# Optimization experiments

Hardware: AMD Instinct MI355X
Metric: run time of the kernel (lower is better)

Reference implementation:

```python
import jax, jax.numpy as jnp
import numpy as np

NUM_HEADS = 8


def setup_inputs() -> dict:
    key = jax.random.key(0)
    ks = jax.random.split(key, 16)
    B, Ct, Co, H, W = 1, 256, 128, 64, 64
    s = lambda k, *shape: jax.random.normal(k, shape, dtype=jnp.float32) * 0.02
    return {
        "thermal_features": jax.random.normal(ks[0], (B, Ct, H, W), dtype=jnp.float32),
        "optical_features": jax.random.normal(ks[1], (B, Co, H, W), dtype=jnp.float32),
        "emissivity_map": jax.random.uniform(ks[2], (B, 1, H, W), dtype=jnp.float32),
        "Wq": s(ks[3], Ct, Ct), "bq": jnp.zeros((Ct,), jnp.float32),
        "Wk": s(ks[4], Ct, Co), "bk": jnp.zeros((Ct,), jnp.float32),
        "Wv": s(ks[5], Ct, Co), "bv": jnp.zeros((Ct,), jnp.float32),
        "conv1_w": s(ks[6], 32, 1, 3, 3), "conv1_b": jnp.zeros((32,), jnp.float32),
        "conv2_w": s(ks[7], NUM_HEADS, 32, 1, 1), "conv2_b": jnp.zeros((NUM_HEADS,), jnp.float32),
        "Wp": s(ks[8], Ct, Ct), "bp": jnp.zeros((Ct,), jnp.float32),
    }


def reference(thermal_features, optical_features, emissivity_map,
              Wq, bq, Wk, bk, Wv, bv, conv1_w, conv1_b, conv2_w, conv2_b, Wp, bp):
    B, Ct, H, W = thermal_features.shape
    Co = optical_features.shape[1]
    N = H * W
    h = NUM_HEADS
    d = Ct // h
    scale = d ** (-0.5)

    # flatten spatial -> tokens: [B, N, C]
    t_flat = thermal_features.reshape(B, Ct, N).transpose(0, 2, 1)
    o_flat = optical_features.reshape(B, Co, N).transpose(0, 2, 1)

    # projections, split heads: [B, h, N, d]
    q = (t_flat @ Wq.T + bq).reshape(B, N, h, d).transpose(0, 2, 1, 3)
    k = (o_flat @ Wk.T + bk).reshape(B, N, h, d).transpose(0, 2, 1, 3)
    v = (o_flat @ Wv.T + bv).reshape(B, N, h, d).transpose(0, 2, 1, 3)

    # full attention scores: [B, h, N, N]
    attn = jnp.einsum('bhqd,bhkd->bhqk', q, k) * scale

    # emissivity gate: Conv(1->32, 3x3, pad 1) -> ReLU -> Conv(32->h, 1x1) -> Sigmoid
    g = jax.lax.conv_general_dilated(emissivity_map, conv1_w, (1, 1), 'SAME',
                                     dimension_numbers=('NCHW', 'OIHW', 'NCHW'))
    g = jax.nn.relu(g + conv1_b[None, :, None, None])
    g = jax.lax.conv_general_dilated(g, conv2_w, (1, 1), 'SAME',
                                     dimension_numbers=('NCHW', 'OIHW', 'NCHW'))
    g = jax.nn.sigmoid(g + conv2_b[None, :, None, None])  # [B, h, H, W]
    g = g.reshape(B, h, N)[..., None]  # [B, h, N, 1] gates query rows

    attn = jax.nn.softmax(attn * g, axis=-1)  # dropout is identity in eval

    out = jnp.einsum('bhqk,bhkd->bhqd', attn, v)  # [B, h, N, d]
    out = out.transpose(0, 2, 1, 3).reshape(B, N, Ct)
    out = out @ Wp.T + bp
    return out.transpose(0, 2, 1).reshape(B, Ct, H, W)
```

## Files before the change

### kernel.cpp

```cpp
#include <hip/hip_runtime.h>
#include <hip/hip_bf16.h>

#define N_TOK 4096
#define CT 256

typedef __attribute__((ext_vector_type(8))) short bf16x8;
typedef __attribute__((ext_vector_type(16))) float f32x16;

__device__ __forceinline__ unsigned pkbf(float a, float b) {
  float2 t; t.x = a; t.y = b;
  __hip_bfloat162 h = __float22bfloat162_rn(t);
  return *reinterpret_cast<unsigned*>(&h);
}

#if __has_builtin(__builtin_amdgcn_exp2f)
__device__ __forceinline__ float fexp2(float x) { return __builtin_amdgcn_exp2f(x); }
#else
__device__ __forceinline__ float fexp2(float x) { return exp2f(x); }
#endif

__global__ __launch_bounds__(256) void prep_kernel(
    const float* __restrict__ thermal, const float* __restrict__ optical,
    const float* __restrict__ Wq, const float* __restrict__ Wk,
    const float* __restrict__ Wv, const float* __restrict__ Wp,
    const float* __restrict__ em, const float* __restrict__ w1,
    const float* __restrict__ b1, const float* __restrict__ w2,
    const float* __restrict__ b2,
    unsigned short* __restrict__ Xbt, unsigned short* __restrict__ Xbo,
    unsigned short* __restrict__ Wall, float* __restrict__ g)
{
  __shared__ unsigned short tile[64][264];
  const int bx = blockIdx.x, tid = threadIdx.x;
  if (bx < 128) {
    const bool th = (bx < 64);
    const float* X = th ? thermal : optical;
    unsigned short* Xb = th ? Xbt : Xbo;
    const int CIN = th ? 256 : 128;
    const int n0 = (th ? bx : bx - 64) * 64;
    const int nl = tid & 63;
    const int cw = (tid >> 6) * 4;
    for (int c0 = 0; c0 < CIN; c0 += 16) {
      int c = c0 + cw;
      float x0 = X[(size_t)(c + 0) * N_TOK + n0 + nl];
      float x1 = X[(size_t)(c + 1) * N_TOK + n0 + nl];
      float x2 = X[(size_t)(c + 2) * N_TOK + n0 + nl];
      float x3 = X[(size_t)(c + 3) * N_TOK + n0 + nl];
      uint2 w; w.x = pkbf(x0, x1); w.y = pkbf(x2, x3);
      *(uint2*)&tile[nl][c] = w;
    }
    __syncthreads();
    const int n = tid >> 2, q = tid & 3;
    const int cb = q * (CIN / 4);
    for (int j = 0; j < CIN / 4; j += 4)
      *(uint2*)(Xb + (size_t)(n0 + n) * CIN + cb + j) = *(const uint2*)&tile[n][cb + j];
  } else if (bx < 224) {
    int i = (bx - 128) * 2048 + tid * 8;
    const float* src; int off;
    if (i < 65536)       { src = Wq; off = 0; }
    else if (i < 98304)  { src = Wk; off = 65536; }
    else if (i < 131072) { src = Wv; off = 98304; }
    else                 { src = Wp; off = 131072; }
    float4 f0 = *(const float4*)(src + (i - off));
    float4 f1 = *(const float4*)(src + (i - off) + 4);
    uint4 o;
    o.x = pkbf(f0.x, f0.y); o.y = pkbf(f0.z, f0.w);
    o.z = pkbf(f1.x, f1.y); o.w = pkbf(f1.z, f1.w);
    *(uint4*)(Wall + i) = o;
  } else {
    int n = (bx - 224) * 256 + tid;
    int y = n >> 6, x = n & 63;
    float e[9];
#pragma unroll
    for (int dy = 0; dy < 3; dy++)
#pragma unroll
      for (int dx = 0; dx < 3; dx++) {
        int yy = y + dy - 1, xx = x + dx - 1;
        e[dy * 3 + dx] = (yy >= 0 && yy < 64 && xx >= 0 && xx < 64)
                             ? em[yy * 64 + xx] : 0.f;
      }
    float c1[32];
#pragma unroll
    for (int oc = 0; oc < 32; oc++) {
      float a = b1[oc];
#pragma unroll
      for (int t = 0; t < 9; t++) a = fmaf(e[t], w1[oc * 9 + t], a);
      c1[oc] = fmaxf(a, 0.f);
    }
#pragma unroll
    for (int hh = 0; hh < 8; hh++) {
      float a = b2[hh];
#pragma unroll
      for (int oc = 0; oc < 32; oc++) a = fmaf(c1[oc], w2[hh * 32 + oc], a);
      g[hh * N_TOK + n] = 1.f / (1.f + __expf(-a));
    }
  }
}

template <int CIN>
__device__ __forceinline__ void gemm_tile(
    const unsigned short* __restrict__ xp, const unsigned short* __restrict__ wp,
    f32x16& accE, f32x16& accO)
{
#pragma unroll
  for (int c = 0; c < CIN; c += 32) {
    bf16x8 a0 = *(const bf16x8*)(xp + c);
    bf16x8 b0 = *(const bf16x8*)(wp + c);
    bf16x8 a1 = *(const bf16x8*)(xp + c + 16);
    bf16x8 b1 = *(const bf16x8*)(wp + c + 16);
    accE = __builtin_amdgcn_mfma_f32_32x32x16_bf16(a0, b0, accE, 0, 0, 0);
    accO = __builtin_amdgcn_mfma_f32_32x32x16_bf16(a1, b1, accO, 0, 0, 0);
  }
}

__global__ __launch_bounds__(256) void qkv_kernel(
    const unsigned short* __restrict__ Xbt, const unsigned short* __restrict__ Xbo,
    const unsigned short* __restrict__ Wall,
    const float* __restrict__ bq, const float* __restrict__ bk,
    const float* __restrict__ bv, const float* __restrict__ g,
    unsigned short* __restrict__ Qh, unsigned short* __restrict__ Kh,
    unsigned short* __restrict__ Vf)
{
  __shared__ float ldsT[4][32][33];
  const int tid = threadIdx.x;
  const int wave = tid >> 6, lane = tid & 63;
  const int l31 = lane & 31, hi = lane >> 5;
  const int y = blockIdx.y;
  const int head = y & 7;
  const int n0 = blockIdx.x * 128 + wave * 32;

  f32x16 accE, accO;
#pragma unroll
  for (int i = 0; i < 16; i++) { accE[i] = 0.f; accO[i] = 0.f; }
  float bo;
  if (y < 8) {
    gemm_tile<256>(Xbt + (size_t)(n0 + l31) * 256 + hi * 8,
                   Wall + (size_t)(head * 32 + l31) * 256 + hi * 8, accE, accO);
    bo = bq[head * 32 + l31];
  } else if (y < 16) {
    gemm_tile<128>(Xbo + (size_t)(n0 + l31) * 128 + hi * 8,
                   Wall + 65536 + (size_t)(head * 32 + l31) * 128 + hi * 8, accE, accO);
    bo = bk[head * 32 + l31];
  } else {
    gemm_tile<128>(Xbo + (size_t)(n0 + l31) * 128 + hi * 8,
                   Wall + 98304 + (size_t)(head * 32 + l31) * 128 + hi * 8, accE, accO);
    bo = bv[head * 32 + l31];
  }
  float val[16];
#pragma unroll
  for (int r = 0; r < 16; r++) val[r] = accE[r] + accO[r] + bo;

  if (y < 8) {
    const float QSC = 0.17677669529663689f * 1.4426950408889634f;
#pragma unroll
    for (int r = 0; r < 16; r++) {
      int t = n0 + (r & 3) + 8 * (r >> 2) + 4 * hi;
      val[r] *= QSC * g[head * N_TOK + t];
    }
  }
#pragma unroll
  for (int r = 0; r < 16; r++)
    ldsT[wave][(r & 3) + 8 * (r >> 2) + 4 * hi][l31] = val[r];

  if (y < 16) {
    unsigned pk[8];
#pragma unroll
    for (int i = 0; i < 8; i++)
      pk[i] = pkbf(ldsT[wave][l31][16 * hi + 2 * i],
                   ldsT[wave][l31][16 * hi + 2 * i + 1]);
    unsigned short* dst = (y < 8 ? Qh : Kh) +
        ((size_t)head * N_TOK + n0 + l31) * 32 + 16 * hi;
    *(uint4*)dst = make_uint4(pk[0], pk[1], pk[2], pk[3]);
    *(uint4*)(dst + 8) = make_uint4(pk[4], pk[5], pk[6], pk[7]);
  } else {
    unsigned pk[8];
#pragma unroll
    for (int i = 0; i < 8; i++)
      pk[i] = pkbf(ldsT[wave][16 * hi + 2 * i][l31],
                   ldsT[wave][16 * hi + 2 * i + 1][l31]);
    unsigned short* dst = Vf +
        (((size_t)head * 256 + (n0 >> 4) + hi) * 32 + l31) * 16;
    *(uint4*)dst = make_uint4(pk[0], pk[1], pk[2], pk[3]);
    *(uint4*)(dst + 8) = make_uint4(pk[4], pk[5], pk[6], pk[7]);
  }
}

__global__ __launch_bounds__(256, 4) void attn_kernel(
    const unsigned short* __restrict__ Qh, const unsigned short* __restrict__ Kh,
    const unsigned short* __restrict__ Vf, unsigned short* __restrict__ Ab)
{
  __shared__ float combA[4][32][33];
  __shared__ float combL[4][32];
  const int tid = threadIdx.x;
  const int wave = tid >> 6, lane = tid & 63;
  const int l31 = lane & 31, hi = lane >> 5;
  const int hh = blockIdx.x >> 7;
  const int qb = blockIdx.x & 127;
  const int qrow0 = qb * 32;
  const int kbase0 = wave * 1024;

  const unsigned short* qrow = Qh + ((size_t)hh * N_TOK + qrow0 + l31) * 32;
  const bf16x8 qf0 = *(const bf16x8*)(qrow + hi * 8);
  const bf16x8 qf1 = *(const bf16x8*)(qrow + 16 + hi * 8);

  const unsigned short* kb_base = Kh + (size_t)hh * (N_TOK * 32);
  const unsigned short* vf_base = Vf + (size_t)hh * (256 * 32 * 16);

  f32x16 acc, zero16;
#pragma unroll
  for (int i = 0; i < 16; i++) { acc[i] = 0.f; zero16[i] = 0.f; }
  float lsum = 0.f;

#define LK(kb, s) (*(const bf16x8*)(kb_base + (size_t)((kb) + l31) * 32 + (s) * 16 + hi * 8))
#define LV(kt2)   (*(const bf16x8*)(vf_base + (size_t)((kt2) * 32 + l31) * 16 + hi * 8))

  bf16x8 kf0 = LK(kbase0, 0), kf1 = LK(kbase0, 1);
  bf16x8 vb0 = LV(kbase0 >> 4), vb1 = LV((kbase0 >> 4) + 1);

#pragma unroll 2
  for (int kt = 0; kt < 1024; kt += 32) {
    const int nxt = (kt + 32 < 1024) ? (kbase0 + kt + 32) : kbase0;
    bf16x8 nk0 = LK(nxt, 0), nk1 = LK(nxt, 1);
    bf16x8 nv0 = LV(nxt >> 4), nv1 = LV((nxt >> 4) + 1);

    f32x16 s = __builtin_amdgcn_mfma_f32_32x32x16_bf16(kf0, qf0, zero16, 0, 0, 0);
    s = __builtin_amdgcn_mfma_f32_32x32x16_bf16(kf1, qf1, s, 0, 0, 0);

    float p[16];
#pragma unroll
    for (int r = 0; r < 16; r++) p[r] = fexp2(s[r]);

    lsum += (((p[0] + p[1]) + (p[2] + p[3])) + ((p[4] + p[5]) + (p[6] + p[7]))) +
            (((p[8] + p[9]) + (p[10] + p[11])) + ((p[12] + p[13]) + (p[14] + p[15])));

    unsigned a0 = pkbf(p[0], p[1]),   a1 = pkbf(p[2], p[3]);
    unsigned b0 = pkbf(p[4], p[5]),   b1 = pkbf(p[6], p[7]);
    unsigned c0 = pkbf(p[8], p[9]),   c1 = pkbf(p[10], p[11]);
    unsigned d0 = pkbf(p[12], p[13]), d1 = pkbf(p[14], p[15]);
    asm("v_permlane32_swap_b32 %0, %1" : "+v"(a0), "+v"(b0));
    asm("v_permlane32_swap_b32 %0, %1" : "+v"(a1), "+v"(b1));
    asm("v_permlane32_swap_b32 %0, %1" : "+v"(c0), "+v"(d0));
    asm("v_permlane32_swap_b32 %0, %1" : "+v"(c1), "+v"(d1));
    union { unsigned w[4]; bf16x8 v; } u0, u1;
    u0.w[0] = a0; u0.w[1] = a1; u0.w[2] = b0; u0.w[3] = b1;
    u1.w[0] = c0; u1.w[1] = c1; u1.w[2] = d0; u1.w[3] = d1;

    acc = __builtin_amdgcn_mfma_f32_32x32x16_bf16(u0.v, vb0, acc, 0, 0, 0);
    acc = __builtin_amdgcn_mfma_f32_32x32x16_bf16(u1.v, vb1, acc, 0, 0, 0);

    kf0 = nk0; kf1 = nk1; vb0 = nv0; vb1 = nv1;
  }
#undef LK
#undef LV

  float lt = lsum + __shfl_xor(lsum, 32);
  if (hi == 0) combL[wave][l31] = lt;

#pragma unroll
  for (int r = 0; r < 16; r++)
    combA[wave][(r & 3) + 8 * (r >> 2) + 4 * hi][l31] = acc[r];
  __syncthreads();

  const int t = tid >> 3;
  const int c4 = (tid & 7) * 4;
  float l = combL[0][t] + combL[1][t] + combL[2][t] + combL[3][t];
  float inv = 1.f / l;
  float o[4];
#pragma unroll
  for (int j = 0; j < 4; j++)
    o[j] = combA[0][t][c4 + j] + combA[1][t][c4 + j] +
           combA[2][t][c4 + j] + combA[3][t][c4 + j];
  uint2 pk;
  pk.x = pkbf(o[0] * inv, o[1] * inv);
  pk.y = pkbf(o[2] * inv, o[3] * inv);
  *(uint2*)(Ab + (size_t)(qrow0 + t) * CT + hh * 32 + c4) = pk;
}

__global__ __launch_bounds__(256) void pout_kernel(
    const unsigned short* __restrict__ Ab, const unsigned short* __restrict__ Wall,
    const float* __restrict__ bp, float* __restrict__ out)
{
  const int tid = threadIdx.x;
  const int wave = tid >> 6, lane = tid & 63;
  const int l31 = lane & 31, hi = lane >> 5;
  const int n0 = blockIdx.x * 128 + wave * 32;
  const int o0 = blockIdx.y * 32;

  f32x16 accE, accO;
#pragma unroll
  for (int i = 0; i < 16; i++) { accE[i] = 0.f; accO[i] = 0.f; }
  gemm_tile<256>(Ab + (size_t)(n0 + l31) * 256 + hi * 8,
                 Wall + 131072 + (size_t)(o0 + l31) * 256 + hi * 8, accE, accO);
  const float bo = bp[o0 + l31];
#pragma unroll
  for (int rr = 0; rr < 4; rr++) {
    float4 w = make_float4(accE[4 * rr + 0] + accO[4 * rr + 0] + bo,
                           accE[4 * rr + 1] + accO[4 * rr + 1] + bo,
                           accE[4 * rr + 2] + accO[4 * rr + 2] + bo,
                           accE[4 * rr + 3] + accO[4 * rr + 3] + bo);
    *(float4*)(out + (size_t)(o0 + l31) * N_TOK + n0 + 8 * rr + 4 * hi) = w;
  }
}

extern "C" void kernel_launch(void* const* d_in, const int* in_sizes, int n_in,
                              void* d_out, int out_size, void* d_ws, size_t ws_size,
                              hipStream_t stream)
{
  const float* thermal = (const float*)d_in[0];
  const float* optical = (const float*)d_in[1];
  const float* em      = (const float*)d_in[2];
  const float* Wq = (const float*)d_in[3];
  const float* bq = (const float*)d_in[4];
  const float* Wk = (const float*)d_in[5];
  const float* bk = (const float*)d_in[6];
  const float* Wv = (const float*)d_in[7];
  const float* bv = (const float*)d_in[8];
  const float* w1 = (const float*)d_in[9];
  const float* b1 = (const float*)d_in[10];
  const float* w2 = (const float*)d_in[11];
  const float* b2 = (const float*)d_in[12];
  const float* Wp = (const float*)d_in[13];
  const float* bp = (const float*)d_in[14];

  char* ws = (char*)d_ws;
  const size_t MB = 1u << 20;
  unsigned short* Xbt = (unsigned short*)(ws);
  unsigned short* Xbo = (unsigned short*)(ws + 2 * MB);
  unsigned short* Wall = (unsigned short*)(ws + 3 * MB);
  float* gbuf = (float*)(ws + 3 * MB + 512 * 1024);
  unsigned short* Qh = (unsigned short*)(ws + 4 * MB);
  unsigned short* Kh = (unsigned short*)(ws + 6 * MB);
  unsigned short* Vf = (unsigned short*)(ws + 8 * MB);
  unsigned short* Ab = (unsigned short*)(ws + 10 * MB);

  prep_kernel<<<240, 256, 0, stream>>>(thermal, optical, Wq, Wk, Wv, Wp,
                                       em, w1, b1, w2, b2, Xbt, Xbo, Wall, gbuf);
  qkv_kernel<<<dim3(32, 24), 256, 0, stream>>>(Xbt, Xbo, Wall, bq, bk, bv, gbuf,
                                               Qh, Kh, Vf);
  attn_kernel<<<1024, 256, 0, stream>>>(Qh, Kh, Vf, Ab);
  pout_kernel<<<dim3(32, 8), 256, 0, stream>>>(Ab, Wall, bp, (float*)d_out);
}
```

Before: 67.69 us.

## Split attention key range across two blocks and merge partials in projection

The attention kernel now splits the 4096 keys into two halves along a new grid dimension, doubling the block count. Each block writes unnormalized fp32 partial outputs and row sums to workspace. The output projection kernel adds the two partials, normalizes by the combined sum, and converts to bf16 before the MFMA. This raises parallelism and shortens each block's serial loop, at the cost of extra fp32 global traffic (two 4 MB partial buffers) and heavier loads in the projection kernel.

```diff
diff --git a/kernel.cpp b/kernel.cpp
--- a/kernel.cpp
+++ b/kernel.cpp
@@ -186,7 +186,8 @@
 
 __global__ __launch_bounds__(256, 4) void attn_kernel(
     const unsigned short* __restrict__ Qh, const unsigned short* __restrict__ Kh,
-    const unsigned short* __restrict__ Vf, unsigned short* __restrict__ Ab)
+    const unsigned short* __restrict__ Vf,
+    float* __restrict__ Abf, float* __restrict__ Lb)
 {
   __shared__ float combA[4][32][33];
   __shared__ float combL[4][32];
@@ -195,8 +196,9 @@
   const int l31 = lane & 31, hi = lane >> 5;
   const int hh = blockIdx.x >> 7;
   const int qb = blockIdx.x & 127;
+  const int split = blockIdx.y;
   const int qrow0 = qb * 32;
-  const int kbase0 = wave * 1024;
+  const int kbase0 = split * 2048 + wave * 512;
 
   const unsigned short* qrow = Qh + ((size_t)hh * N_TOK + qrow0 + l31) * 32;
   const bf16x8 qf0 = *(const bf16x8*)(qrow + hi * 8);
@@ -217,8 +219,8 @@
   bf16x8 vb0 = LV(kbase0 >> 4), vb1 = LV((kbase0 >> 4) + 1);
 
 #pragma unroll 2
-  for (int kt = 0; kt < 1024; kt += 32) {
-    const int nxt = (kt + 32 < 1024) ? (kbase0 + kt + 32) : kbase0;
+  for (int kt = 0; kt < 512; kt += 32) {
+    const int nxt = (kt + 32 < 512) ? (kbase0 + kt + 32) : kbase0;
     bf16x8 nk0 = LK(nxt, 0), nk1 = LK(nxt, 1);
     bf16x8 nv0 = LV(nxt >> 4), nv1 = LV((nxt >> 4) + 1);
 
@@ -262,34 +264,70 @@
 
   const int t = tid >> 3;
   const int c4 = (tid & 7) * 4;
-  float l = combL[0][t] + combL[1][t] + combL[2][t] + combL[3][t];
-  float inv = 1.f / l;
   float o[4];
 #pragma unroll
   for (int j = 0; j < 4; j++)
     o[j] = combA[0][t][c4 + j] + combA[1][t][c4 + j] +
            combA[2][t][c4 + j] + combA[3][t][c4 + j];
-  uint2 pk;
-  pk.x = pkbf(o[0] * inv, o[1] * inv);
-  pk.y = pkbf(o[2] * inv, o[3] * inv);
-  *(uint2*)(Ab + (size_t)(qrow0 + t) * CT + hh * 32 + c4) = pk;
+  *(float4*)(Abf + ((size_t)split * N_TOK + qrow0 + t) * CT + hh * 32 + c4) =
+      make_float4(o[0], o[1], o[2], o[3]);
+  if ((tid & 7) == 0) {
+    float l = combL[0][t] + combL[1][t] + combL[2][t] + combL[3][t];
+    Lb[((size_t)split * 8 + hh) * N_TOK + qrow0 + t] = l;
+  }
 }
 
 __global__ __launch_bounds__(256) void pout_kernel(
-    const unsigned short* __restrict__ Ab, const unsigned short* __restrict__ Wall,
-    const float* __restrict__ bp, float* __restrict__ out)
+    const float* __restrict__ Abf, const float* __restrict__ Lb,
+    const unsigned short* __restrict__ Wall, const float* __restrict__ bp,
+    float* __restrict__ out)
 {
   const int tid = threadIdx.x;
   const int wave = tid >> 6, lane = tid & 63;
   const int l31 = lane & 31, hi = lane >> 5;
   const int n0 = blockIdx.x * 128 + wave * 32;
   const int o0 = blockIdx.y * 32;
+  const int token = n0 + l31;
+
+  float invl[8];
+#pragma unroll
+  for (int h = 0; h < 8; h++)
+    invl[h] = 1.f / (Lb[(size_t)h * N_TOK + token] +
+                     Lb[(size_t)(8 + h) * N_TOK + token]);
+
+  const float* A0 = Abf + (size_t)token * CT;
+  const float* A1 = Abf + (size_t)(N_TOK + token) * CT;
 
   f32x16 accE, accO;
 #pragma unroll
   for (int i = 0; i < 16; i++) { accE[i] = 0.f; accO[i] = 0.f; }
-  gemm_tile<256>(Ab + (size_t)(n0 + l31) * 256 + hi * 8,
-                 Wall + 131072 + (size_t)(o0 + l31) * 256 + hi * 8, accE, accO);
+  const unsigned short* wp = Wall + 131072 + (size_t)(o0 + l31) * 256 + hi * 8;
+
+#pragma unroll
+  for (int c = 0; c < 256; c += 32) {
+    const float il = invl[c >> 5];
+    float4 x0a = *(const float4*)(A0 + c + hi * 8);
+    float4 x0b = *(const float4*)(A0 + c + hi * 8 + 4);
+    float4 y0a = *(const float4*)(A1 + c + hi * 8);
+    float4 y0b = *(const float4*)(A1 + c + hi * 8 + 4);
+    float4 x1a = *(const float4*)(A0 + c + 16 + hi * 8);
+    float4 x1b = *(const float4*)(A0 + c + 16 + hi * 8 + 4);
+    float4 y1a = *(const float4*)(A1 + c + 16 + hi * 8);
+    float4 y1b = *(const float4*)(A1 + c + 16 + hi * 8 + 4);
+    union { unsigned w[4]; bf16x8 v; } a0u, a1u;
+    a0u.w[0] = pkbf((x0a.x + y0a.x) * il, (x0a.y + y0a.y) * il);
+    a0u.w[1] = pkbf((x0a.z + y0a.z) * il, (x0a.w + y0a.w) * il);
+    a0u.w[2] = pkbf((x0b.x + y0b.x) * il, (x0b.y + y0b.y) * il);
+    a0u.w[3] = pkbf((x0b.z + y0b.z) * il, (x0b.w + y0b.w) * il);
+    a1u.w[0] = pkbf((x1a.x + y1a.x) * il, (x1a.y + y1a.y) * il);
+    a1u.w[1] = pkbf((x1a.z + y1a.z) * il, (x1a.w + y1a.w) * il);
+    a1u.w[2] = pkbf((x1b.x + y1b.x) * il, (x1b.y + y1b.y) * il);
+    a1u.w[3] = pkbf((x1b.z + y1b.z) * il, (x1b.w + y1b.w) * il);
+    bf16x8 b0 = *(const bf16x8*)(wp + c);
+    bf16x8 b1 = *(const bf16x8*)(wp + c + 16);
+    accE = __builtin_amdgcn_mfma_f32_32x32x16_bf16(a0u.v, b0, accE, 0, 0, 0);
+    accO = __builtin_amdgcn_mfma_f32_32x32x16_bf16(a1u.v, b1, accO, 0, 0, 0);
+  }
   const float bo = bp[o0 + l31];
 #pragma unroll
   for (int rr = 0; rr < 4; rr++) {
@@ -330,12 +368,13 @@
   unsigned short* Qh = (unsigned short*)(ws + 4 * MB);
   unsigned short* Kh = (unsigned short*)(ws + 6 * MB);
   unsigned short* Vf = (unsigned short*)(ws + 8 * MB);
-  unsigned short* Ab = (unsigned short*)(ws + 10 * MB);
+  float* Abf = (float*)(ws + 10 * MB);
+  float* Lb  = (float*)(ws + 18 * MB);
 
   prep_kernel<<<240, 256, 0, stream>>>(thermal, optical, Wq, Wk, Wv, Wp,
                                        em, w1, b1, w2, b2, Xbt, Xbo, Wall, gbuf);
   qkv_kernel<<<dim3(32, 24), 256, 0, stream>>>(Xbt, Xbo, Wall, bq, bk, bv, gbuf,
                                                Qh, Kh, Vf);
-  attn_kernel<<<1024, 256, 0, stream>>>(Qh, Kh, Vf, Ab);
-  pout_kernel<<<dim3(32, 8), 256, 0, stream>>>(Ab, Wall, bp, (float*)d_out);
-}
+  attn_kernel<<<dim3(1024, 2), 256, 0, stream>>>(Qh, Kh, Vf, Abf, Lb);
+  pout_kernel<<<dim3(32, 8), 256, 0, stream>>>(Abf, Lb, Wall, bp, (float*)d_out);
+}
```

Result: slower. 78.43 us (+15.9%).
